# Kernel optimization log

Hardware: AMD Instinct MI355X
Metric: run time of the kernel (lower is better)

The kernel has to match this reference:

```python
import jax, jax.numpy as jnp
import numpy as np

N_OSC = 32
CONV = 1000.0  # convergence_factor


def _cpg_ode(y, ia, ifr, cw, pb):
    # Faithful to CPGOde.forward, including its unpacking order:
    # (amplitudes, amplitudes_dot, phases) = (y[:n], y[n:2n], y[2n:3n])
    n = N_OSC
    a = y[:n]
    a_dot = y[n:2 * n]
    ph = y[2 * n:3 * n]
    phase_dots = ifr + jnp.sum(a[:, None] * cw * jnp.sin(ph[None, :] - ph[:, None] - pb), axis=1)
    a_dd = CONV * (CONV / 4.0 * (ia - a) - a_dot)
    # states_to_tensor(amplitudes_dot, phase_dots, amplitudes_dot_dot)
    return jnp.concatenate([a_dot, phase_dots, a_dd])


def _rk4_38_step(f, y, h):
    # torchdiffeq 'rk4' = rk4_alt_step_func (3/8 rule), one step over t=[0, h]
    k1 = f(y)
    k2 = f(y + h * k1 / 3.0)
    k3 = f(y + h * (k2 - k1 / 3.0))
    k4 = f(y + h * (k1 - k2 + k3))
    return y + h * 0.125 * (k1 + 3.0 * (k2 + k3) + k4)


def _mlp(x, Ws, bs):
    # Linear stack with ReLU between layers, none after the last
    for i, (W, b) in enumerate(zip(Ws, bs)):
        x = W @ x + b
        if i < len(Ws) - 1:
            x = jax.nn.relu(x)
    return x


def _init_linear(key, fan_in, fan_out):
    kW, kb = jax.random.split(key)
    bound = 1.0 / np.sqrt(fan_in)
    W = jax.random.uniform(kW, (fan_out, fan_in), minval=-bound, maxval=bound, dtype=jnp.float32)
    b = jax.random.uniform(kb, (fan_out,), minval=-bound, maxval=bound, dtype=jnp.float32)
    return W, b


def setup_inputs() -> dict:
    key = jax.random.key(0)
    ks = jax.random.split(key, 10)
    n = N_OSC
    n_params = 2 * n + 2 * n * n  # 2112
    in_dims = [2049, 4096, 4096, n_params]  # input_layers[0]+1, ..., final param layer
    out_dims = [2 * n, 2048, 2048, 1024]
    inp = {}
    inp["state"] = jax.random.normal(ks[0], (3 * n,), dtype=jnp.float32) * 0.1
    inp["x"] = jax.random.normal(ks[1], (2048,), dtype=jnp.float32)
    inp["timestep"] = jnp.array(0.01, dtype=jnp.float32)
    for i in range(3):
        W, b = _init_linear(ks[2 + i], in_dims[i], in_dims[i + 1])
        inp[f"in_W{i}"] = W
        inp[f"in_b{i}"] = b
    for i in range(3):
        W, b = _init_linear(ks[5 + i], out_dims[i], out_dims[i + 1])
        inp[f"out_W{i}"] = W
        inp[f"out_b{i}"] = b
    return inp


def reference(state, x, timestep,
              in_W0, in_b0, in_W1, in_b1, in_W2, in_b2,
              out_W0, out_b0, out_W1, out_b1, out_W2, out_b2):
    n = N_OSC
    # append timestep scalar to the input features
    x = jnp.concatenate([x, timestep[None]])
    params = _mlp(x, [in_W0, in_W1, in_W2], [in_b0, in_b1, in_b2])
    ia = params[:n]
    ifr = params[n:2 * n]
    cw = params[2 * n:2 * n + n * n].reshape(n, n)
    pb = params[2 * n + n * n:].reshape(n, n)
    f = lambda y: _cpg_ode(y, ia, ifr, cw, pb)
    new_state = _rk4_38_step(f, state, timestep)
    a = new_state[:n]
    ph = new_state[n:2 * n]
    cpg_out = jnp.concatenate([a * jnp.cos(ph), a * jnp.sin(ph)])
    out = _mlp(cpg_out, [out_W0, out_W1, out_W2], [out_b0, out_b1, out_b2])
    return (jax.lax.stop_gradient(new_state), out)
```

## Files before the change

kernel.cpp:

```cpp
#include <hip/hip_runtime.h>
#include <stdint.h>

template<int RELU, int TSCOL>
__global__ __launch_bounds__(256) void gemv_k(
    const float* __restrict__ W, const float* __restrict__ B,
    const float* __restrict__ x, const float* __restrict__ ts,
    float* __restrict__ y, int rows, int cols)
{
    int wv   = threadIdx.x >> 6;
    int lane = threadIdx.x & 63;
    int row  = blockIdx.x * 4 + wv;
    if (row >= rows) return;

    int n = TSCOL ? cols - 1 : cols;
    const float* w = W + (size_t)row * (size_t)cols;
    float sum = 0.0f;

    int mis = (int)(((uintptr_t)w >> 2) & 3);
    int start = (4 - mis) & 3;
    if (start > n) start = n;
    if (lane < start) sum += w[lane] * x[lane];
    int nv = (n - start) >> 2;
    const float4* wp = (const float4*)(w + start);
    const float* xs = x + start;
    int g = lane;
    for (; g + 448 < nv; g += 512) {
        float4 u0 = wp[g];
        float4 u1 = wp[g + 64];
        float4 u2 = wp[g + 128];
        float4 u3 = wp[g + 192];
        float4 u4 = wp[g + 256];
        float4 u5 = wp[g + 320];
        float4 u6 = wp[g + 384];
        float4 u7 = wp[g + 448];
        const float* x0 = xs + 4 * g;
        sum += u0.x * x0[0]    + u0.y * x0[1]    + u0.z * x0[2]    + u0.w * x0[3];
        sum += u1.x * x0[256]  + u1.y * x0[257]  + u1.z * x0[258]  + u1.w * x0[259];
        sum += u2.x * x0[512]  + u2.y * x0[513]  + u2.z * x0[514]  + u2.w * x0[515];
        sum += u3.x * x0[768]  + u3.y * x0[769]  + u3.z * x0[770]  + u3.w * x0[771];
        sum += u4.x * x0[1024] + u4.y * x0[1025] + u4.z * x0[1026] + u4.w * x0[1027];
        sum += u5.x * x0[1280] + u5.y * x0[1281] + u5.z * x0[1282] + u5.w * x0[1283];
        sum += u6.x * x0[1536] + u6.y * x0[1537] + u6.z * x0[1538] + u6.w * x0[1539];
        sum += u7.x * x0[1792] + u7.y * x0[1793] + u7.z * x0[1794] + u7.w * x0[1795];
    }
    for (; g < nv; g += 64) {
        float4 u = wp[g];
        const float* xp = xs + 4 * g;
        sum += u.x * xp[0] + u.y * xp[1] + u.z * xp[2] + u.w * xp[3];
    }
    int t = start + nv * 4 + lane;
    if (t < n) sum += w[t] * x[t];
    if (TSCOL && lane == 0) sum += w[n] * ts[0];

    #pragma unroll
    for (int off = 32; off > 0; off >>= 1) sum += __shfl_down(sum, off);

    if (lane == 0) {
        float r = sum + B[row];
        if (RELU) r = fmaxf(r, 0.0f);
        y[row] = r;
    }
}

template<int RELU>
__global__ __launch_bounds__(256) void gemv2_k(
    const float* __restrict__ W, const float* __restrict__ B,
    const float* __restrict__ x, float* __restrict__ y, int cols)
{
    int gw   = blockIdx.x * 4 + (threadIdx.x >> 6);
    int lane = threadIdx.x & 63;
    int r0 = gw * 2;

    const float4* w0p = (const float4*)(W + (size_t)r0 * (size_t)cols);
    const float4* w1p = (const float4*)(W + (size_t)(r0 + 1) * (size_t)cols);
    const float4* xp  = (const float4*)x;
    int nv = cols >> 2;

    float s0 = 0.0f, s1 = 0.0f;
    int g = lane;
    for (; g + 192 < nv; g += 256) {
        float4 xv0 = xp[g];       float4 a0 = w0p[g];       float4 b0 = w1p[g];
        float4 xv1 = xp[g + 64];  float4 a1 = w0p[g + 64];  float4 b1 = w1p[g + 64];
        float4 xv2 = xp[g + 128]; float4 a2 = w0p[g + 128]; float4 b2 = w1p[g + 128];
        float4 xv3 = xp[g + 192]; float4 a3 = w0p[g + 192]; float4 b3 = w1p[g + 192];
        s0 += a0.x*xv0.x + a0.y*xv0.y + a0.z*xv0.z + a0.w*xv0.w;
        s1 += b0.x*xv0.x + b0.y*xv0.y + b0.z*xv0.z + b0.w*xv0.w;
        s0 += a1.x*xv1.x + a1.y*xv1.y + a1.z*xv1.z + a1.w*xv1.w;
        s1 += b1.x*xv1.x + b1.y*xv1.y + b1.z*xv1.z + b1.w*xv1.w;
        s0 += a2.x*xv2.x + a2.y*xv2.y + a2.z*xv2.z + a2.w*xv2.w;
        s1 += b2.x*xv2.x + b2.y*xv2.y + b2.z*xv2.z + b2.w*xv2.w;
        s0 += a3.x*xv3.x + a3.y*xv3.y + a3.z*xv3.z + a3.w*xv3.w;
        s1 += b3.x*xv3.x + b3.y*xv3.y + b3.z*xv3.z + b3.w*xv3.w;
    }
    for (; g < nv; g += 64) {
        float4 xv = xp[g];
        float4 a = w0p[g];
        float4 b = w1p[g];
        s0 += a.x*xv.x + a.y*xv.y + a.z*xv.z + a.w*xv.w;
        s1 += b.x*xv.x + b.y*xv.y + b.z*xv.z + b.w*xv.w;
    }

    #pragma unroll
    for (int off = 32; off > 0; off >>= 1) {
        s0 += __shfl_down(s0, off);
        s1 += __shfl_down(s1, off);
    }
    if (lane == 0) {
        float v0 = s0 + B[r0];
        float v1 = s1 + B[r0 + 1];
        if (RELU) { v0 = fmaxf(v0, 0.0f); v1 = fmaxf(v1, 0.0f); }
        y[r0]     = v0;
        y[r0 + 1] = v1;
    }
}

__global__ __launch_bounds__(256) void ode_ow0_k(
    const float* __restrict__ state, const float* __restrict__ ts,
    const float* __restrict__ params,
    const float* __restrict__ oW0, const float* __restrict__ ob0,
    float* __restrict__ g0, float* __restrict__ out_state)
{
    const float CONV = 1000.0f;
    __shared__ float s_cw[32 * 33];
    __shared__ float s_spb[32 * 33];
    __shared__ float s_cpb[32 * 33];
    __shared__ float s_s[32], s_c[32];
    __shared__ float s_cpg[64];
    int tid = threadIdx.x;

    for (int k = tid; k < 1024; k += 256) {
        int p = k + (k >> 5);
        s_cw[p] = params[64 + k];
        float sp, cp;
        sincosf(params[1088 + k], &sp, &cp);
        s_spb[p] = sp;
        s_cpb[p] = cp;
    }
    __syncthreads();

    bool act = (tid < 32);
    int i = tid;
    float ia = 0.f, ifr = 0.f, y0a = 0.f, y0b = 0.f, y0c = 0.f;
    if (act) {
        ia  = params[i];
        ifr = params[32 + i];
        y0a = state[i];
        y0b = state[32 + i];
        y0c = state[64 + i];
    }
    float h = ts[0];

    float k1a=0,k1b=0,k1c=0, k2a=0,k2b=0,k2c=0, k3a=0,k3b=0,k3c=0, k4a=0,k4b=0,k4c=0;

    auto do_eval = [&](float a, float ad, float ph,
                       float& fa, float& fb, float& fc) {
        __syncthreads();
        if (act) {
            float s, c;
            sincosf(ph, &s, &c);
            s_s[i] = s; s_c[i] = c;
        }
        __syncthreads();
        if (act) {
            float si = s_s[i], ci = s_c[i];
            float ssum = 0.0f;
            #pragma unroll
            for (int j = 0; j < 32; j++) {
                float sj = s_s[j], cj = s_c[j];
                float sdp = sj * ci - cj * si;
                float cdp = cj * ci + sj * si;
                int p = i * 33 + j;
                float sv = sdp * s_cpb[p] - cdp * s_spb[p];
                ssum += s_cw[p] * sv;
            }
            fa = ad;
            fb = ifr + a * ssum;
            fc = CONV * (CONV * 0.25f * (ia - a) - ad);
        }
    };

    do_eval(y0a, y0b, y0c, k1a, k1b, k1c);
    do_eval(y0a + h * k1a / 3.0f,
            y0b + h * k1b / 3.0f,
            y0c + h * k1c / 3.0f, k2a, k2b, k2c);
    do_eval(y0a + h * (k2a - k1a / 3.0f),
            y0b + h * (k2b - k1b / 3.0f),
            y0c + h * (k2c - k1c / 3.0f), k3a, k3b, k3c);
    do_eval(y0a + h * (k1a - k2a + k3a),
            y0b + h * (k1b - k2b + k3b),
            y0c + h * (k1c - k2c + k3c), k4a, k4b, k4c);

    if (act) {
        float na = y0a + h * 0.125f * (k1a + 3.0f * (k2a + k3a) + k4a);
        float nb = y0b + h * 0.125f * (k1b + 3.0f * (k2b + k3b) + k4b);
        float nc = y0c + h * 0.125f * (k1c + 3.0f * (k2c + k3c) + k4c);
        if (blockIdx.x == 0) {
            out_state[i]      = na;
            out_state[32 + i] = nb;
            out_state[64 + i] = nc;
        }
        s_cpg[i]      = na * cosf(nb);
        s_cpg[32 + i] = na * sinf(nb);
    }
    __syncthreads();

    int wv   = tid >> 6;
    int lane = tid & 63;
    int row  = blockIdx.x * 4 + wv;
    float sum = oW0[(size_t)row * 64 + lane] * s_cpg[lane];
    #pragma unroll
    for (int off = 32; off > 0; off >>= 1) sum += __shfl_down(sum, off);
    if (lane == 0) g0[row] = fmaxf(sum + ob0[row], 0.0f);
}

extern "C" void kernel_launch(void* const* d_in, const int* in_sizes, int n_in,
                              void* d_out, int out_size, void* d_ws, size_t ws_size,
                              hipStream_t stream) {
    const float* state = (const float*)d_in[0];
    const float* x     = (const float*)d_in[1];
    const float* ts    = (const float*)d_in[2];
    const float* inW0  = (const float*)d_in[3];
    const float* inb0  = (const float*)d_in[4];
    const float* inW1  = (const float*)d_in[5];
    const float* inb1  = (const float*)d_in[6];
    const float* inW2  = (const float*)d_in[7];
    const float* inb2  = (const float*)d_in[8];
    const float* oW0   = (const float*)d_in[9];
    const float* ob0   = (const float*)d_in[10];
    const float* oW1   = (const float*)d_in[11];
    const float* ob1   = (const float*)d_in[12];
    const float* oW2   = (const float*)d_in[13];
    const float* ob2   = (const float*)d_in[14];

    float* ws  = (float*)d_ws;
    float* h0  = ws;
    float* h1  = ws + 4096;
    float* pr  = ws + 8192;
    float* g0  = ws + 10368;
    float* g1  = ws + 12416;

    float* out = (float*)d_out;

    gemv_k<1,1><<<1024, 256, 0, stream>>>(inW0, inb0, x, ts, h0, 4096, 2049);
    gemv2_k<1><<<512, 256, 0, stream>>>(inW1, inb1, h0, h1, 4096);
    gemv2_k<0><<<264, 256, 0, stream>>>(inW2, inb2, h1, pr, 4096);
    ode_ow0_k<<<512, 256, 0, stream>>>(state, ts, pr, oW0, ob0, g0, out);
    gemv2_k<1><<<256, 256, 0, stream>>>(oW1, ob1, g0, g1, 2048);
    gemv2_k<0><<<128, 256, 0, stream>>>(oW2, ob2, g1, out + 96, 2048);
}
```

Before: 215.2 us.

## Fuse whole MLP-ODE-MLP pipeline into one cooperative persistent kernel with grid syncs

Replaces the six separate kernel launches with a single cooperative kernel of 512 blocks that runs every GEMV stage and the RK4 ODE step, with grid.sync between stages. Each block redoes the ODE redundantly in shared memory, precomputing sin/cos of the phase biases so each evaluation uses angle-difference identities instead of per-pair sincos. The aim is to remove launch gaps and inter-kernel drain/fill bubbles. The cost is grid-wide barriers and fixed occupancy, and the old launches remain as a fallback if the cooperative launch fails.

Result: slower. 472.0 us (+119.3%).

```diff
diff --git a/kernel.cpp b/kernel.cpp
--- a/kernel.cpp
+++ b/kernel.cpp
@@ -1,5 +1,257 @@
 #include <hip/hip_runtime.h>
+#include <hip/hip_cooperative_groups.h>
 #include <stdint.h>
+
+namespace cg = cooperative_groups;
+
+__device__ __forceinline__ float wave_reduce(float s) {
+    #pragma unroll
+    for (int off = 32; off > 0; off >>= 1) s += __shfl_down(s, off);
+    return s;
+}
+
+__device__ __forceinline__ float dot_row_aligned(const float* __restrict__ w,
+                                                 const float* __restrict__ xv,
+                                                 int cols, int lane) {
+    const float4* wp = (const float4*)w;
+    const float4* xp = (const float4*)xv;
+    int nv = cols >> 2;
+    float s = 0.0f;
+    int g = lane;
+    for (; g + 192 < nv; g += 256) {
+        float4 x0 = xp[g];       float4 a0 = wp[g];
+        float4 x1 = xp[g + 64];  float4 a1 = wp[g + 64];
+        float4 x2 = xp[g + 128]; float4 a2 = wp[g + 128];
+        float4 x3 = xp[g + 192]; float4 a3 = wp[g + 192];
+        s += a0.x*x0.x + a0.y*x0.y + a0.z*x0.z + a0.w*x0.w;
+        s += a1.x*x1.x + a1.y*x1.y + a1.z*x1.z + a1.w*x1.w;
+        s += a2.x*x2.x + a2.y*x2.y + a2.z*x2.z + a2.w*x2.w;
+        s += a3.x*x3.x + a3.y*x3.y + a3.z*x3.z + a3.w*x3.w;
+    }
+    for (; g < nv; g += 64) {
+        float4 xq = xp[g]; float4 a = wp[g];
+        s += a.x*xq.x + a.y*xq.y + a.z*xq.z + a.w*xq.w;
+    }
+    return s;
+}
+
+__global__ __launch_bounds__(256, 2) void fused_k(
+    const float* __restrict__ state, const float* __restrict__ x,
+    const float* __restrict__ ts,
+    const float* __restrict__ inW0, const float* __restrict__ inb0,
+    const float* __restrict__ inW1, const float* __restrict__ inb1,
+    const float* __restrict__ inW2, const float* __restrict__ inb2,
+    const float* __restrict__ oW0, const float* __restrict__ ob0,
+    const float* __restrict__ oW1, const float* __restrict__ ob1,
+    const float* __restrict__ oW2, const float* __restrict__ ob2,
+    float* __restrict__ h0, float* __restrict__ h1, float* __restrict__ pr,
+    float* __restrict__ g0, float* __restrict__ g1, float* __restrict__ out)
+{
+    const float CONV = 1000.0f;
+    __shared__ float s_cw[32 * 33];
+    __shared__ float s_spb[32 * 33];
+    __shared__ float s_cpb[32 * 33];
+    __shared__ float s_s[32], s_c[32];
+    __shared__ float s_cpg[64];
+
+    cg::grid_group grid = cg::this_grid();
+    int tid  = threadIdx.x;
+    int wv   = tid >> 6;
+    int lane = tid & 63;
+    int gw   = blockIdx.x * 4 + wv;
+
+    {
+        const float* w0 = inW0 + (size_t)gw * 2049;
+        const float* w1 = inW0 + (size_t)(gw + 2048) * 2049;
+        const int n = 2048;
+        float s0 = 0.0f, s1 = 0.0f;
+        int mis = (int)(((uintptr_t)w0 >> 2) & 3);
+        int start = (4 - mis) & 3;
+        if (lane < start) { float xv = x[lane]; s0 += w0[lane] * xv; s1 += w1[lane] * xv; }
+        int nv = (n - start) >> 2;
+        const float4* w0p = (const float4*)(w0 + start);
+        const float4* w1p = (const float4*)(w1 + start);
+        const float* xs = x + start;
+        int g = lane;
+        for (; g + 192 < nv; g += 256) {
+            float4 a0 = w0p[g];       float4 b0 = w1p[g];
+            float4 a1 = w0p[g + 64];  float4 b1 = w1p[g + 64];
+            float4 a2 = w0p[g + 128]; float4 b2 = w1p[g + 128];
+            float4 a3 = w0p[g + 192]; float4 b3 = w1p[g + 192];
+            const float* xq = xs + 4 * g;
+            s0 += a0.x*xq[0]   + a0.y*xq[1]   + a0.z*xq[2]   + a0.w*xq[3];
+            s1 += b0.x*xq[0]   + b0.y*xq[1]   + b0.z*xq[2]   + b0.w*xq[3];
+            s0 += a1.x*xq[256] + a1.y*xq[257] + a1.z*xq[258] + a1.w*xq[259];
+            s1 += b1.x*xq[256] + b1.y*xq[257] + b1.z*xq[258] + b1.w*xq[259];
+            s0 += a2.x*xq[512] + a2.y*xq[513] + a2.z*xq[514] + a2.w*xq[515];
+            s1 += b2.x*xq[512] + b2.y*xq[513] + b2.z*xq[514] + b2.w*xq[515];
+            s0 += a3.x*xq[768] + a3.y*xq[769] + a3.z*xq[770] + a3.w*xq[771];
+            s1 += b3.x*xq[768] + b3.y*xq[769] + b3.z*xq[770] + b3.w*xq[771];
+        }
+        for (; g < nv; g += 64) {
+            float4 a = w0p[g]; float4 b = w1p[g];
+            const float* xq = xs + 4 * g;
+            s0 += a.x*xq[0] + a.y*xq[1] + a.z*xq[2] + a.w*xq[3];
+            s1 += b.x*xq[0] + b.y*xq[1] + b.z*xq[2] + b.w*xq[3];
+        }
+        int t = start + nv * 4 + lane;
+        if (t < n) { float xv = x[t]; s0 += w0[t] * xv; s1 += w1[t] * xv; }
+        if (lane == 0) { float tv = ts[0]; s0 += w0[n] * tv; s1 += w1[n] * tv; }
+        s0 = wave_reduce(s0);
+        s1 = wave_reduce(s1);
+        if (lane == 0) {
+            h0[gw]        = fmaxf(s0 + inb0[gw], 0.0f);
+            h0[gw + 2048] = fmaxf(s1 + inb0[gw + 2048], 0.0f);
+        }
+    }
+    grid.sync();
+
+    {
+        const float4* w0p = (const float4*)(inW1 + (size_t)gw * 4096);
+        const float4* w1p = (const float4*)(inW1 + (size_t)(gw + 2048) * 4096);
+        const float4* xp  = (const float4*)h0;
+        float s0 = 0.0f, s1 = 0.0f;
+        int g = lane;
+        for (; g + 192 < 1024; g += 256) {
+            float4 xv0 = xp[g];       float4 a0 = w0p[g];       float4 b0 = w1p[g];
+            float4 xv1 = xp[g + 64];  float4 a1 = w0p[g + 64];  float4 b1 = w1p[g + 64];
+            float4 xv2 = xp[g + 128]; float4 a2 = w0p[g + 128]; float4 b2 = w1p[g + 128];
+            float4 xv3 = xp[g + 192]; float4 a3 = w0p[g + 192]; float4 b3 = w1p[g + 192];
+            s0 += a0.x*xv0.x + a0.y*xv0.y + a0.z*xv0.z + a0.w*xv0.w;
+            s1 += b0.x*xv0.x + b0.y*xv0.y + b0.z*xv0.z + b0.w*xv0.w;
+            s0 += a1.x*xv1.x + a1.y*xv1.y + a1.z*xv1.z + a1.w*xv1.w;
+            s1 += b1.x*xv1.x + b1.y*xv1.y + b1.z*xv1.z + b1.w*xv1.w;
+            s0 += a2.x*xv2.x + a2.y*xv2.y + a2.z*xv2.z + a2.w*xv2.w;
+            s1 += b2.x*xv2.x + b2.y*xv2.y + b2.z*xv2.z + b2.w*xv2.w;
+            s0 += a3.x*xv3.x + a3.y*xv3.y + a3.z*xv3.z + a3.w*xv3.w;
+            s1 += b3.x*xv3.x + b3.y*xv3.y + b3.z*xv3.z + b3.w*xv3.w;
+        }
+        for (; g < 1024; g += 64) {
+            float4 xv = xp[g]; float4 a = w0p[g]; float4 b = w1p[g];
+            s0 += a.x*xv.x + a.y*xv.y + a.z*xv.z + a.w*xv.w;
+            s1 += b.x*xv.x + b.y*xv.y + b.z*xv.z + b.w*xv.w;
+        }
+        s0 = wave_reduce(s0);
+        s1 = wave_reduce(s1);
+        if (lane == 0) {
+            h1[gw]        = fmaxf(s0 + inb1[gw], 0.0f);
+            h1[gw + 2048] = fmaxf(s1 + inb1[gw + 2048], 0.0f);
+        }
+    }
+    grid.sync();
+
+    {
+        float s = dot_row_aligned(inW2 + (size_t)gw * 4096, h1, 4096, lane);
+        s = wave_reduce(s);
+        if (lane == 0) pr[gw] = s + inb2[gw];
+        if ((gw & 31) == 0) {
+            int r = 2048 + (gw >> 5);
+            float s2 = dot_row_aligned(inW2 + (size_t)r * 4096, h1, 4096, lane);
+            s2 = wave_reduce(s2);
+            if (lane == 0) pr[r] = s2 + inb2[r];
+        }
+    }
+    grid.sync();
+
+    for (int k = tid; k < 1024; k += 256) {
+        int p = k + (k >> 5);
+        s_cw[p] = pr[64 + k];
+        float sp, cp;
+        sincosf(pr[1088 + k], &sp, &cp);
+        s_spb[p] = sp;
+        s_cpb[p] = cp;
+    }
+    __syncthreads();
+
+    {
+        bool act = (tid < 32);
+        int i = tid;
+        float ia = 0.f, ifr = 0.f, y0a = 0.f, y0b = 0.f, y0c = 0.f;
+        if (act) {
+            ia  = pr[i];
+            ifr = pr[32 + i];
+            y0a = state[i];
+            y0b = state[32 + i];
+            y0c = state[64 + i];
+        }
+        float h = ts[0];
+
+        float k1a=0,k1b=0,k1c=0, k2a=0,k2b=0,k2c=0, k3a=0,k3b=0,k3c=0, k4a=0,k4b=0,k4c=0;
+
+        auto do_eval = [&](float a, float ad, float ph,
+                           float& fa, float& fb, float& fc) {
+            __syncthreads();
+            if (act) {
+                float s, c;
+                sincosf(ph, &s, &c);
+                s_s[i] = s; s_c[i] = c;
+            }
+            __syncthreads();
+            if (act) {
+                float si = s_s[i], ci = s_c[i];
+                float ssum = 0.0f;
+                #pragma unroll
+                for (int j = 0; j < 32; j++) {
+                    float sj = s_s[j], cj = s_c[j];
+                    float sdp = sj * ci - cj * si;
+                    float cdp = cj * ci + sj * si;
+                    int p = i * 33 + j;
+                    float sv = sdp * s_cpb[p] - cdp * s_spb[p];
+                    ssum += s_cw[p] * sv;
+                }
+                fa = ad;
+                fb = ifr + a * ssum;
+                fc = CONV * (CONV * 0.25f * (ia - a) - ad);
+            }
+        };
+
+        do_eval(y0a, y0b, y0c, k1a, k1b, k1c);
+        do_eval(y0a + h * k1a / 3.0f,
+                y0b + h * k1b / 3.0f,
+                y0c + h * k1c / 3.0f, k2a, k2b, k2c);
+        do_eval(y0a + h * (k2a - k1a / 3.0f),
+                y0b + h * (k2b - k1b / 3.0f),
+                y0c + h * (k2c - k1c / 3.0f), k3a, k3b, k3c);
+        do_eval(y0a + h * (k1a - k2a + k3a),
+                y0b + h * (k1b - k2b + k3b),
+                y0c + h * (k1c - k2c + k3c), k4a, k4b, k4c);
+
+        if (act) {
+            float na = y0a + h * 0.125f * (k1a + 3.0f * (k2a + k3a) + k4a);
+            float nb = y0b + h * 0.125f * (k1b + 3.0f * (k2b + k3b) + k4b);
+            float nc = y0c + h * 0.125f * (k1c + 3.0f * (k2c + k3c) + k4c);
+            if (blockIdx.x == 0) {
+                out[i]      = na;
+                out[32 + i] = nb;
+                out[64 + i] = nc;
+            }
+            s_cpg[i]      = na * cosf(nb);
+            s_cpg[32 + i] = na * sinf(nb);
+        }
+    }
+    __syncthreads();
+
+    {
+        float sum = oW0[(size_t)gw * 64 + lane] * s_cpg[lane];
+        sum = wave_reduce(sum);
+        if (lane == 0) g0[gw] = fmaxf(sum + ob0[gw], 0.0f);
+    }
+    grid.sync();
+
+    {
+        float s = dot_row_aligned(oW1 + (size_t)gw * 2048, g0, 2048, lane);
+        s = wave_reduce(s);
+        if (lane == 0) g1[gw] = fmaxf(s + ob1[gw], 0.0f);
+    }
+    grid.sync();
+
+    if ((gw & 1) == 0) {
+        int r = gw >> 1;
+        float s = dot_row_aligned(oW2 + (size_t)r * 2048, g1, 2048, lane);
+        s = wave_reduce(s);
+        if (lane == 0) out[96 + r] = s + ob2[r];
+    }
+}
 
 template<int RELU, int TSCOL>
 __global__ __launch_bounds__(256) void gemv_k(
@@ -241,10 +493,22 @@
 
     float* out = (float*)d_out;
 
-    gemv_k<1,1><<<1024, 256, 0, stream>>>(inW0, inb0, x, ts, h0, 4096, 2049);
-    gemv2_k<1><<<512, 256, 0, stream>>>(inW1, inb1, h0, h1, 4096);
-    gemv2_k<0><<<264, 256, 0, stream>>>(inW2, inb2, h1, pr, 4096);
-    ode_ow0_k<<<512, 256, 0, stream>>>(state, ts, pr, oW0, ob0, g0, out);
-    gemv2_k<1><<<256, 256, 0, stream>>>(oW1, ob1, g0, g1, 2048);
-    gemv2_k<0><<<128, 256, 0, stream>>>(oW2, ob2, g1, out + 96, 2048);
-}
+    void* args[] = {
+        (void*)&state, (void*)&x, (void*)&ts,
+        (void*)&inW0, (void*)&inb0, (void*)&inW1, (void*)&inb1,
+        (void*)&inW2, (void*)&inb2, (void*)&oW0, (void*)&ob0,
+        (void*)&oW1, (void*)&ob1, (void*)&oW2, (void*)&ob2,
+        (void*)&h0, (void*)&h1, (void*)&pr, (void*)&g0, (void*)&g1, (void*)&out
+    };
+    hipError_t err = hipLaunchCooperativeKernel((void*)fused_k, dim3(512), dim3(256),
+                                                args, 0, stream);
+    if (err != hipSuccess) {
+        (void)hipGetLastError();
+        gemv_k<1,1><<<1024, 256, 0, stream>>>(inW0, inb0, x, ts, h0, 4096, 2049);
+        gemv2_k<1><<<512, 256, 0, stream>>>(inW1, inb1, h0, h1, 4096);
+        gemv2_k<0><<<264, 256, 0, stream>>>(inW2, inb2, h1, pr, 4096);
+        ode_ow0_k<<<512, 256, 0, stream>>>(state, ts, pr, oW0, ob0, g0, out);
+        gemv2_k<1><<<256, 256, 0, stream>>>(oW1, ob1, g0, g1, 2048);
+        gemv2_k<0><<<128, 256, 0, stream>>>(oW2, ob2, g1, out + 96, 2048);
+    }
+}
```
